# Kernel tuning notes

Hardware: AMD Instinct MI355X
Metric: run time of the kernel (lower is better)

## Reference

```python
import jax, jax.numpy as jnp
import numpy as np

B, C, H, W = 32, 384, 64, 64
M, R = 64, 16  # token_count, factor_r


def setup_inputs() -> dict:
    key = jax.random.key(0)
    k1, k2, k3, k4 = jax.random.split(key, 4)
    x = jax.random.normal(k1, (B, C, H, W), dtype=jnp.float32)
    # 1x1 conv == per-pixel linear map C -> R
    Vw = jax.random.normal(k2, (R, C), dtype=jnp.float32) * (1.0 / np.sqrt(C))
    Vb = jax.random.normal(k3, (R,), dtype=jnp.float32) * 0.01
    U = jax.random.normal(k4, (M, R), dtype=jnp.float32) * 0.02
    return {"x": x, "Vw": Vw, "Vb": Vb, "U": U}


def reference(x, Vw, Vb, U):
    b, c, h, w = x.shape
    n = h * w
    x_flat = x.reshape(b, c, n)                       # [B,C,N]
    # 1x1 conv projection: [B,R,N]
    V = jnp.einsum('rc,bcn->brn', Vw, x_flat) + Vb[None, :, None]
    # low-rank bilinear logits: [B,M,N]
    L = jnp.einsum('mr,brn->bmn', U, V)
    # softmax over token dim (axis=1), matching F.softmax(L, dim=1)
    S = jax.nn.softmax(L, axis=1)
    # pooled tokens: [B,C,M]
    T = jnp.einsum('bcn,bmn->bcm', x_flat, S)
    return (T, S)
```

## Files before the change

kernel.cpp:

```cpp
#include <hip/hip_runtime.h>
#include <hip/hip_bf16.h>

#define B_ 32
#define C_ 384
#define N_ 4096
#define M_ 64
#define R_ 16

typedef __attribute__((ext_vector_type(8))) short short8;
typedef __attribute__((ext_vector_type(4))) float f32x4;
typedef __attribute__((ext_vector_type(4))) int i32x4;

static __device__ __forceinline__ unsigned short f2bf(float f) {
    union { float f; unsigned u; } v; v.f = f;
    unsigned r = v.u + 0x7fffu + ((v.u >> 16) & 1u);
    return (unsigned short)(r >> 16);
}

__global__ __launch_bounds__(256, 2) void k_logits_softmax(
    const float* __restrict__ x, const float* __restrict__ Vw,
    const float* __restrict__ Vb, const float* __restrict__ U,
    float* __restrict__ S)
{
    __shared__ unsigned short w2s[64][392];
    __shared__ __align__(16) char scratch[28928];
    __shared__ float b2s[64];
    __shared__ float vbs[16];

    float* vws = (float*)scratch;
    float* us  = (float*)(scratch + 24576);
    unsigned short (*xts)[72] = (unsigned short (*)[72])scratch;

    const int t = threadIdx.x;

    {
        const float4* vw4 = (const float4*)Vw;
        #pragma unroll
        for (int i = 0; i < 6; ++i)
            ((float4*)vws)[t + i * 256] = vw4[t + i * 256];
        float4 uv = ((const float4*)U)[t];
        const int um = t >> 2, ur0 = (t & 3) * 4;
        us[um * 17 + ur0 + 0] = uv.x;
        us[um * 17 + ur0 + 1] = uv.y;
        us[um * 17 + ur0 + 2] = uv.z;
        us[um * 17 + ur0 + 3] = uv.w;
        if (t < 16) vbs[t] = Vb[t];
    }
    __syncthreads();
    {
        const int m  = t >> 2;
        const int cg = t & 3;
        float u[R_];
        #pragma unroll
        for (int r = 0; r < R_; ++r) u[r] = us[m * 17 + r];
        if (cg == 0) {
            float a = 0.f;
            #pragma unroll
            for (int r = 0; r < R_; ++r) a = fmaf(u[r], vbs[r], a);
            b2s[m] = a;
        }
        #pragma unroll 4
        for (int j = 0; j < 48; ++j) {
            const int c = cg * 2 + j * 8;
            float a0 = 0.f, a1 = 0.f;
            #pragma unroll
            for (int r = 0; r < R_; ++r) {
                float2 vv = *(const float2*)(vws + r * C_ + c);
                a0 = fmaf(u[r], vv.x, a0);
                a1 = fmaf(u[r], vv.y, a1);
            }
            unsigned pk = (unsigned)f2bf(a0) | ((unsigned)f2bf(a1) << 16);
            *(unsigned*)&w2s[m][c] = pk;
        }
    }
    __syncthreads();

    const int b    = blockIdx.x >> 5;
    const int n0   = (blockIdx.x & 31) * 128;
    const int lane = t & 63, q = lane >> 4, col = lane & 15;
    const int w    = t >> 6;

    f32x4 acc[4][2];
    #pragma unroll
    for (int mt = 0; mt < 4; ++mt)
        #pragma unroll
        for (int nt = 0; nt < 2; ++nt)
            acc[mt][nt] = (f32x4){0.f, 0.f, 0.f, 0.f};

    const float* xbase = x + (size_t)(b * C_) * N_ + n0 + 2 * lane;

    for (int kc = 0; kc < 12; ++kc) {
        unsigned wA[4], wB[4];
        const float* xp = xbase + (size_t)(kc * 32 + w * 8) * N_;
        #pragma unroll
        for (int i = 0; i < 8; ++i) {
            float2 v = *(const float2*)(xp + (size_t)i * N_);
            unsigned ba = f2bf(v.x), bb = f2bf(v.y);
            if ((i & 1) == 0) { wA[i >> 1] = ba;        wB[i >> 1] = bb; }
            else              { wA[i >> 1] |= ba << 16; wB[i >> 1] |= bb << 16; }
        }
        __syncthreads();
        {
            const int nl = 2 * lane;
            i32x4 pa = {(int)wA[0], (int)wA[1], (int)wA[2], (int)wA[3]};
            i32x4 pb = {(int)wB[0], (int)wB[1], (int)wB[2], (int)wB[3]};
            *(i32x4*)&xts[nl][w * 8]     = pa;
            *(i32x4*)&xts[nl + 1][w * 8] = pb;
        }
        __syncthreads();

        short8 af[4], bfr[2];
        #pragma unroll
        for (int mt = 0; mt < 4; ++mt)
            af[mt] = *(const short8*)&w2s[mt * 16 + col][kc * 32 + q * 8];
        #pragma unroll
        for (int nt = 0; nt < 2; ++nt)
            bfr[nt] = *(const short8*)&xts[w * 32 + nt * 16 + col][q * 8];
        #pragma unroll
        for (int mt = 0; mt < 4; ++mt)
            #pragma unroll
            for (int nt = 0; nt < 2; ++nt)
                acc[mt][nt] = __builtin_amdgcn_mfma_f32_16x16x32_bf16(
                    af[mt], bfr[nt], acc[mt][nt], 0, 0, 0);
    }

    float bias[4][4];
    #pragma unroll
    for (int mt = 0; mt < 4; ++mt)
        #pragma unroll
        for (int r = 0; r < 4; ++r)
            bias[mt][r] = b2s[mt * 16 + q * 4 + r];

    float* Sb = S + (size_t)(b * M_) * N_ + n0 + w * 32 + col;
    #pragma unroll
    for (int nt = 0; nt < 2; ++nt) {
        float mx = -3.4e38f;
        #pragma unroll
        for (int mt = 0; mt < 4; ++mt)
            #pragma unroll
            for (int r = 0; r < 4; ++r) {
                float v = acc[mt][nt][r] + bias[mt][r];
                acc[mt][nt][r] = v;
                mx = fmaxf(mx, v);
            }
        mx = fmaxf(mx, __shfl_xor(mx, 16, 64));
        mx = fmaxf(mx, __shfl_xor(mx, 32, 64));
        float sm = 0.f;
        #pragma unroll
        for (int mt = 0; mt < 4; ++mt)
            #pragma unroll
            for (int r = 0; r < 4; ++r) {
                float e = __expf(acc[mt][nt][r] - mx);
                acc[mt][nt][r] = e;
                sm += e;
            }
        sm += __shfl_xor(sm, 16, 64);
        sm += __shfl_xor(sm, 32, 64);
        const float inv = 1.0f / sm;
        #pragma unroll
        for (int mt = 0; mt < 4; ++mt)
            #pragma unroll
            for (int r = 0; r < 4; ++r)
                Sb[(size_t)(mt * 16 + q * 4 + r) * N_ + nt * 16] = acc[mt][nt][r] * inv;
    }
}

__global__ __launch_bounds__(256, 3) void k_pool2(
    const float* __restrict__ x, const float* __restrict__ S,
    float* __restrict__ T)
{
    __shared__ unsigned short xls[64][72];
    __shared__ unsigned short sls[64][72];

    const int t  = threadIdx.x;
    const int ct = blockIdx.x;
    const int b  = blockIdx.y;
    const int nq = blockIdx.z;
    const int c0 = ct * 64;

    const int rl = t >> 2;
    const int ns = (t & 3) * 16;

    const float* xp = x + (size_t)(b * C_ + c0 + rl) * N_ + nq * 1024 + ns;
    const float* sp = S + (size_t)(b * M_ + rl) * N_ + nq * 1024 + ns;

    const int lane = t & 63, q = lane >> 4, col = lane & 15;
    const int w    = t >> 6;

    f32x4 acc[4];
    #pragma unroll
    for (int mt = 0; mt < 4; ++mt) acc[mt] = (f32x4){0.f, 0.f, 0.f, 0.f};

    for (int kc = 0; kc < 16; ++kc) {
        float4 xv[4], sv[4];
        #pragma unroll
        for (int u = 0; u < 4; ++u) {
            xv[u] = *(const float4*)(xp + kc * 64 + u * 4);
            sv[u] = *(const float4*)(sp + kc * 64 + u * 4);
        }
        unsigned wx[8], ws[8];
        #pragma unroll
        for (int u = 0; u < 4; ++u) {
            wx[u*2]   = (unsigned)f2bf(xv[u].x) | ((unsigned)f2bf(xv[u].y) << 16);
            wx[u*2+1] = (unsigned)f2bf(xv[u].z) | ((unsigned)f2bf(xv[u].w) << 16);
            ws[u*2]   = (unsigned)f2bf(sv[u].x) | ((unsigned)f2bf(sv[u].y) << 16);
            ws[u*2+1] = (unsigned)f2bf(sv[u].z) | ((unsigned)f2bf(sv[u].w) << 16);
        }
        __syncthreads();
        {
            i32x4 p0 = {(int)wx[0], (int)wx[1], (int)wx[2], (int)wx[3]};
            i32x4 p1 = {(int)wx[4], (int)wx[5], (int)wx[6], (int)wx[7]};
            i32x4 p2 = {(int)ws[0], (int)ws[1], (int)ws[2], (int)ws[3]};
            i32x4 p3 = {(int)ws[4], (int)ws[5], (int)ws[6], (int)ws[7]};
            *(i32x4*)&xls[rl][ns]     = p0;
            *(i32x4*)&xls[rl][ns + 8] = p1;
            *(i32x4*)&sls[rl][ns]     = p2;
            *(i32x4*)&sls[rl][ns + 8] = p3;
        }
        __syncthreads();

        #pragma unroll
        for (int ks = 0; ks < 2; ++ks) {
            short8 af = *(const short8*)&xls[w * 16 + col][ks * 32 + q * 8];
            #pragma unroll
            for (int mt = 0; mt < 4; ++mt) {
                short8 bfr = *(const short8*)&sls[mt * 16 + col][ks * 32 + q * 8];
                acc[mt] = __builtin_amdgcn_mfma_f32_16x16x32_bf16(af, bfr, acc[mt], 0, 0, 0);
            }
        }
    }

    float* Tb = T + (size_t)b * C_ * M_;
    #pragma unroll
    for (int mt = 0; mt < 4; ++mt)
        #pragma unroll
        for (int r = 0; r < 4; ++r)
            atomicAdd(&Tb[(size_t)(c0 + w * 16 + q * 4 + r) * M_ + mt * 16 + col],
                      acc[mt][r]);
}

extern "C" void kernel_launch(void* const* d_in, const int* in_sizes, int n_in,
                              void* d_out, int out_size, void* d_ws, size_t ws_size,
                              hipStream_t stream) {
    const float* x  = (const float*)d_in[0];
    const float* Vw = (const float*)d_in[1];
    const float* Vb = (const float*)d_in[2];
    const float* U  = (const float*)d_in[3];
    float* T = (float*)d_out;
    float* S = (float*)d_out + (size_t)B_ * C_ * M_;

    hipMemsetAsync(T, 0, (size_t)B_ * C_ * M_ * sizeof(float), stream);
    k_logits_softmax<<<dim3(32 * 32), dim3(256), 0, stream>>>(x, Vw, Vb, U, S);
    k_pool2<<<dim3(6, 32, 4), dim3(256), 0, stream>>>(x, S, T);
}
```

Measured before the change: 369.1 us.

## Precompute fused U·Vw weights once and enlarge pool kernel channel tile

```diff
diff --git a/kernel.cpp b/kernel.cpp
--- a/kernel.cpp
+++ b/kernel.cpp
@@ -17,63 +17,64 @@
     return (unsigned short)(r >> 16);
 }
 
+__global__ __launch_bounds__(256) void k_w2(
+    const float* __restrict__ Vw, const float* __restrict__ Vb,
+    const float* __restrict__ U, unsigned short* __restrict__ W2,
+    float* __restrict__ b2)
+{
+    __shared__ float vws[16 * 384];
+    __shared__ float vbs[16];
+    const int t = threadIdx.x;
+
+    #pragma unroll
+    for (int j = 0; j < 6; ++j)
+        ((float4*)vws)[t + j * 256] = ((const float4*)Vw)[t + j * 256];
+    if (t < 16) vbs[t] = Vb[t];
+    __syncthreads();
+
+    const int m  = blockIdx.x * 8 + (t >> 5);
+    const int cg = t & 31;
+    float u[R_];
+    #pragma unroll
+    for (int r = 0; r < R_; ++r) u[r] = U[m * R_ + r];
+    if (cg == 0) {
+        float a = 0.f;
+        #pragma unroll
+        for (int r = 0; r < R_; ++r) a = fmaf(u[r], vbs[r], a);
+        b2[m] = a;
+    }
+    #pragma unroll
+    for (int j = 0; j < 6; ++j) {
+        const int c = cg * 2 + j * 64;
+        float a0 = 0.f, a1 = 0.f;
+        #pragma unroll
+        for (int r = 0; r < R_; ++r) {
+            float2 vv = *(const float2*)(vws + r * C_ + c);
+            a0 = fmaf(u[r], vv.x, a0);
+            a1 = fmaf(u[r], vv.y, a1);
+        }
+        unsigned pk = (unsigned)f2bf(a0) | ((unsigned)f2bf(a1) << 16);
+        *(unsigned*)&W2[m * C_ + c] = pk;
+    }
+}
+
 __global__ __launch_bounds__(256, 2) void k_logits_softmax(
-    const float* __restrict__ x, const float* __restrict__ Vw,
-    const float* __restrict__ Vb, const float* __restrict__ U,
-    float* __restrict__ S)
+    const float* __restrict__ x, const unsigned short* __restrict__ W2,
+    const float* __restrict__ b2, float* __restrict__ S)
 {
     __shared__ unsigned short w2s[64][392];
-    __shared__ __align__(16) char scratch[28928];
+    __shared__ unsigned short xts[128][72];
     __shared__ float b2s[64];
-    __shared__ float vbs[16];
-
-    float* vws = (float*)scratch;
-    float* us  = (float*)(scratch + 24576);
-    unsigned short (*xts)[72] = (unsigned short (*)[72])scratch;
 
     const int t = threadIdx.x;
 
-    {
-        const float4* vw4 = (const float4*)Vw;
-        #pragma unroll
-        for (int i = 0; i < 6; ++i)
-            ((float4*)vws)[t + i * 256] = vw4[t + i * 256];
-        float4 uv = ((const float4*)U)[t];
-        const int um = t >> 2, ur0 = (t & 3) * 4;
-        us[um * 17 + ur0 + 0] = uv.x;
-        us[um * 17 + ur0 + 1] = uv.y;
-        us[um * 17 + ur0 + 2] = uv.z;
-        us[um * 17 + ur0 + 3] = uv.w;
-        if (t < 16) vbs[t] = Vb[t];
-    }
-    __syncthreads();
-    {
-        const int m  = t >> 2;
-        const int cg = t & 3;
-        float u[R_];
-        #pragma unroll
-        for (int r = 0; r < R_; ++r) u[r] = us[m * 17 + r];
-        if (cg == 0) {
-            float a = 0.f;
-            #pragma unroll
-            for (int r = 0; r < R_; ++r) a = fmaf(u[r], vbs[r], a);
-            b2s[m] = a;
-        }
-        #pragma unroll 4
-        for (int j = 0; j < 48; ++j) {
-            const int c = cg * 2 + j * 8;
-            float a0 = 0.f, a1 = 0.f;
-            #pragma unroll
-            for (int r = 0; r < R_; ++r) {
-                float2 vv = *(const float2*)(vws + r * C_ + c);
-                a0 = fmaf(u[r], vv.x, a0);
-                a1 = fmaf(u[r], vv.y, a1);
-            }
-            unsigned pk = (unsigned)f2bf(a0) | ((unsigned)f2bf(a1) << 16);
-            *(unsigned*)&w2s[m][c] = pk;
-        }
-    }
-    __syncthreads();
+    #pragma unroll
+    for (int j = 0; j < 12; ++j) {
+        int idx = t + j * 256;
+        int m = idx / 48, c8 = idx % 48;
+        *(i32x4*)&w2s[m][c8 * 8] = ((const i32x4*)W2)[idx];
+    }
+    if (t < 64) b2s[t] = b2[t];
 
     const int b    = blockIdx.x >> 5;
     const int n0   = (blockIdx.x & 31) * 128;
@@ -165,78 +166,93 @@
     }
 }
 
-__global__ __launch_bounds__(256, 3) void k_pool2(
+__global__ __launch_bounds__(256, 4) void k_pool2(
     const float* __restrict__ x, const float* __restrict__ S,
     float* __restrict__ T)
 {
-    __shared__ unsigned short xls[64][72];
+    __shared__ unsigned short xls[128][72];
     __shared__ unsigned short sls[64][72];
 
     const int t  = threadIdx.x;
     const int ct = blockIdx.x;
     const int b  = blockIdx.y;
     const int nq = blockIdx.z;
-    const int c0 = ct * 64;
-
-    const int rl = t >> 2;
-    const int ns = (t & 3) * 16;
-
-    const float* xp = x + (size_t)(b * C_ + c0 + rl) * N_ + nq * 1024 + ns;
-    const float* sp = S + (size_t)(b * M_ + rl) * N_ + nq * 1024 + ns;
+    const int c0 = ct * 128;
+
+    const float* xb = x + (size_t)(b * C_ + c0) * N_ + nq * 512;
+    const float* sb = S + (size_t)(b * M_) * N_ + nq * 512;
 
     const int lane = t & 63, q = lane >> 4, col = lane & 15;
     const int w    = t >> 6;
 
-    f32x4 acc[4];
-    #pragma unroll
-    for (int mt = 0; mt < 4; ++mt) acc[mt] = (f32x4){0.f, 0.f, 0.f, 0.f};
-
-    for (int kc = 0; kc < 16; ++kc) {
-        float4 xv[4], sv[4];
-        #pragma unroll
-        for (int u = 0; u < 4; ++u) {
-            xv[u] = *(const float4*)(xp + kc * 64 + u * 4);
-            sv[u] = *(const float4*)(sp + kc * 64 + u * 4);
-        }
-        unsigned wx[8], ws[8];
-        #pragma unroll
-        for (int u = 0; u < 4; ++u) {
-            wx[u*2]   = (unsigned)f2bf(xv[u].x) | ((unsigned)f2bf(xv[u].y) << 16);
-            wx[u*2+1] = (unsigned)f2bf(xv[u].z) | ((unsigned)f2bf(xv[u].w) << 16);
-            ws[u*2]   = (unsigned)f2bf(sv[u].x) | ((unsigned)f2bf(sv[u].y) << 16);
-            ws[u*2+1] = (unsigned)f2bf(sv[u].z) | ((unsigned)f2bf(sv[u].w) << 16);
-        }
-        __syncthreads();
-        {
-            i32x4 p0 = {(int)wx[0], (int)wx[1], (int)wx[2], (int)wx[3]};
-            i32x4 p1 = {(int)wx[4], (int)wx[5], (int)wx[6], (int)wx[7]};
-            i32x4 p2 = {(int)ws[0], (int)ws[1], (int)ws[2], (int)ws[3]};
-            i32x4 p3 = {(int)ws[4], (int)ws[5], (int)ws[6], (int)ws[7]};
-            *(i32x4*)&xls[rl][ns]     = p0;
-            *(i32x4*)&xls[rl][ns + 8] = p1;
-            *(i32x4*)&sls[rl][ns]     = p2;
-            *(i32x4*)&sls[rl][ns + 8] = p3;
+    f32x4 acc[2][4];
+    #pragma unroll
+    for (int i = 0; i < 2; ++i)
+        #pragma unroll
+        for (int mt = 0; mt < 4; ++mt) acc[i][mt] = (f32x4){0.f, 0.f, 0.f, 0.f};
+
+    for (int kc = 0; kc < 8; ++kc) {
+        float4 xv[8], sv[4];
+        #pragma unroll
+        for (int j = 0; j < 8; ++j) {
+            int idx = t + j * 256;
+            int row = idx >> 4, cc = idx & 15;
+            xv[j] = *(const float4*)(xb + (size_t)row * N_ + kc * 64 + cc * 4);
+        }
+        #pragma unroll
+        for (int j = 0; j < 4; ++j) {
+            int idx = t + j * 256;
+            int row = idx >> 4, cc = idx & 15;
+            sv[j] = *(const float4*)(sb + (size_t)row * N_ + kc * 64 + cc * 4);
+        }
+        __syncthreads();
+        #pragma unroll
+        for (int j = 0; j < 8; ++j) {
+            int idx = t + j * 256;
+            int row = idx >> 4, cc = idx & 15;
+            int2 p;
+            p.x = (int)((unsigned)f2bf(xv[j].x) | ((unsigned)f2bf(xv[j].y) << 16));
+            p.y = (int)((unsigned)f2bf(xv[j].z) | ((unsigned)f2bf(xv[j].w) << 16));
+            *(int2*)&xls[row][cc * 4] = p;
+        }
+        #pragma unroll
+        for (int j = 0; j < 4; ++j) {
+            int idx = t + j * 256;
+            int row = idx >> 4, cc = idx & 15;
+            int2 p;
+            p.x = (int)((unsigned)f2bf(sv[j].x) | ((unsigned)f2bf(sv[j].y) << 16));
+            p.y = (int)((unsigned)f2bf(sv[j].z) | ((unsigned)f2bf(sv[j].w) << 16));
+            *(int2*)&sls[row][cc * 4] = p;
         }
         __syncthreads();
 
         #pragma unroll
         for (int ks = 0; ks < 2; ++ks) {
-            short8 af = *(const short8*)&xls[w * 16 + col][ks * 32 + q * 8];
+            short8 af[2];
+            #pragma unroll
+            for (int i = 0; i < 2; ++i)
+                af[i] = *(const short8*)&xls[w * 32 + i * 16 + col][ks * 32 + q * 8];
             #pragma unroll
             for (int mt = 0; mt < 4; ++mt) {
                 short8 bfr = *(const short8*)&sls[mt * 16 + col][ks * 32 + q * 8];
-                acc[mt] = __builtin_amdgcn_mfma_f32_16x16x32_bf16(af, bfr, acc[mt], 0, 0, 0);
+                #pragma unroll
+                for (int i = 0; i < 2; ++i)
+                    acc[i][mt] = __builtin_amdgcn_mfma_f32_16x16x32_bf16(
+                        af[i], bfr, acc[i][mt], 0, 0, 0);
             }
         }
-    }
-
-    float* Tb = T + (size_t)b * C_ * M_;
-    #pragma unroll
-    for (int mt = 0; mt < 4; ++mt)
-        #pragma unroll
-        for (int r = 0; r < 4; ++r)
-            atomicAdd(&Tb[(size_t)(c0 + w * 16 + q * 4 + r) * M_ + mt * 16 + col],
-                      acc[mt][r]);
+        __syncthreads();
+    }
+
+    float* Tb = T + (size_t)b * C_ * M_ + (size_t)c0 * M_;
+    #pragma unroll
+    for (int i = 0; i < 2; ++i)
+        #pragma unroll
+        for (int mt = 0; mt < 4; ++mt)
+            #pragma unroll
+            for (int r = 0; r < 4; ++r)
+                atomicAdd(&Tb[(size_t)(w * 32 + i * 16 + q * 4 + r) * M_ + mt * 16 + col],
+                          acc[i][mt][r]);
 }
 
 extern "C" void kernel_launch(void* const* d_in, const int* in_sizes, int n_in,
@@ -249,7 +265,11 @@
     float* T = (float*)d_out;
     float* S = (float*)d_out + (size_t)B_ * C_ * M_;
 
+    unsigned short* W2 = (unsigned short*)d_ws;
+    float* b2 = (float*)((char*)d_ws + 64 * 384 * 2);
+
     hipMemsetAsync(T, 0, (size_t)B_ * C_ * M_ * sizeof(float), stream);
-    k_logits_softmax<<<dim3(32 * 32), dim3(256), 0, stream>>>(x, Vw, Vb, U, S);
-    k_pool2<<<dim3(6, 32, 4), dim3(256), 0, stream>>>(x, S, T);
-}
+    k_w2<<<dim3(8), dim3(256), 0, stream>>>(Vw, Vb, U, W2, b2);
+    k_logits_softmax<<<dim3(32 * 32), dim3(256), 0, stream>>>(x, W2, b2, S);
+    k_pool2<<<dim3(3, 32, 8), dim3(256), 0, stream>>>(x, S, T);
+}
```

New measurement: 337.5 us. -8.6%, faster.
